# Kernel optimization log

Measured on AMD Instinct MI355X. Metric: run time of the kernel, lower is better.

Reference implementation:

```python
import jax, jax.numpy as jnp
import numpy as np

N, C = 131072, 128
NUM_PREDICTORS = 8


def setup_inputs() -> dict:
    key = jax.random.key(0)
    ks = jax.random.split(key, 9)
    d = {f"outputs{i+1}": jax.random.normal(ks[i], (N, C), dtype=jnp.float32) for i in range(7)}
    d["mimic"] = jax.random.normal(ks[7], (N, C), dtype=jnp.float32)
    d["targets"] = jax.random.randint(ks[8], (N,), 0, C, dtype=jnp.int32)
    d["n_test"] = N
    return d


def _margin(x, targets):
    # x: [N, C]; top-2 margin if the target logit is the max, else 0 (ties by value equality, as in torch code)
    top2, _ = jax.lax.top_k(x, 2)                                  # [N, 2]
    tval = jnp.take_along_axis(x, targets[:, None], axis=1)[:, 0]  # [N]
    return jnp.where(tval == top2[:, 0], top2[:, 0] - top2[:, 1], jnp.zeros((), x.dtype))


def reference(outputs1, outputs2, outputs3, outputs4, outputs5, outputs6, outputs7, mimic, targets, n_test):
    T = 2.0
    preds = [outputs1, outputs2, outputs3, outputs4, outputs5, outputs6, outputs7, mimic]
    # [N, 8] margins, one column per predictor
    margins = jnp.stack([_margin(p, targets) for p in preds], axis=1)
    out_threshold = jax.nn.softmax(margins / T, axis=1)            # softmax over the 8 predictors per sample
    max_preds = jnp.max(jnp.stack(preds[:7], axis=0))              # global max over outputs1..7
    return max_preds, out_threshold
```

## Files before the change

### kernel.cpp

```cpp
#include <hip/hip_runtime.h>
#include <cfloat>

constexpr int kN = 131072;
constexpr int kC = 128;
constexpr int kRows = 16;

__device__ __forceinline__ unsigned fmap(float f) {
    unsigned b = __float_as_uint(f);
    return (b & 0x80000000u) ? ~b : (b | 0x80000000u);
}

__global__ __launch_bounds__(256, 4) void margins_kernel(
    const float* __restrict__ p0, const float* __restrict__ p1,
    const float* __restrict__ p2, const float* __restrict__ p3,
    const float* __restrict__ p4, const float* __restrict__ p5,
    const float* __restrict__ p6, const float* __restrict__ p7,
    const int* __restrict__ targets, float* __restrict__ out,
    unsigned* __restrict__ gmax_ws)
{
    __shared__ float2 P2[8][kRows][34];
    __shared__ float tvbuf[8][17];
    __shared__ float marg[kRows][12];
    __shared__ unsigned blockmax;

    const int t = threadIdx.x;
    const int row0 = blockIdx.x * kRows;
    if (t == 0) blockmax = 0u;

    const float* preds[8] = {p0, p1, p2, p3, p4, p5, p6, p7};

    const int c  = t & 31;
    const int a0 = t >> 5;

#pragma unroll
    for (int it = 0; it < 2; ++it) {
        const int a   = a0 + it * 8;
        const int row = row0 + a;
        const int tgt = targets[row];
        const size_t off = (size_t)row * kC + c * 4;

        float4 v[8];
#pragma unroll
        for (int j = 0; j < 8; ++j) v[j] = *(const float4*)(preds[j] + off);

        const bool hasT = (tgt >> 2) == c;
        const int  ts   = tgt & 3;

#pragma unroll
        for (int j = 0; j < 8; ++j) {
            const float4 w = v[j];
            float a1 = fmaxf(w.x, w.y), a2 = fminf(w.x, w.y);
            float b1 = fmaxf(w.z, w.w), b2 = fminf(w.z, w.w);
            float m1 = fmaxf(a1, b1);
            float m2 = fmaxf(fminf(a1, b1), fmaxf(a2, b2));
            P2[j][a][c] = make_float2(m1, m2);
            if (hasT) {
                float tv = (ts == 0) ? w.x : (ts == 1) ? w.y : (ts == 2) ? w.z : w.w;
                tvbuf[j][a] = tv;
            }
        }
    }
    __syncthreads();

    if (t < 128) {
        const int r = t & 15;
        const int j = t >> 4;
        const float4* pr = (const float4*)(&P2[j][r][0]);
        float m1 = -FLT_MAX, m2 = -FLT_MAX;
#pragma unroll
        for (int k = 0; k < 16; ++k) {
            const float4 q = pr[k];
            float lo = fminf(m1, q.x);
            m1 = fmaxf(m1, q.x);
            m2 = fmaxf(fmaxf(m2, q.y), lo);
            lo = fminf(m1, q.z);
            m1 = fmaxf(m1, q.z);
            m2 = fmaxf(fmaxf(m2, q.w), lo);
        }
        const float tv = tvbuf[j][r];
        marg[r][j] = (tv == m1) ? (m1 - m2) : 0.0f;
        if (j < 7) atomicMax(&blockmax, fmap(m1));
    }
    __syncthreads();

    if (t < 128) {
        const int r  = t >> 3;
        const int jj = t & 7;
        const float4 ma = *(const float4*)&marg[r][0];
        const float4 mb = *(const float4*)&marg[r][4];
        float mm = fmaxf(fmaxf(fmaxf(ma.x, ma.y), fmaxf(ma.z, ma.w)),
                         fmaxf(fmaxf(mb.x, mb.y), fmaxf(mb.z, mb.w)));
        const float e0 = __expf((ma.x - mm) * 0.5f);
        const float e1 = __expf((ma.y - mm) * 0.5f);
        const float e2 = __expf((ma.z - mm) * 0.5f);
        const float e3 = __expf((ma.w - mm) * 0.5f);
        const float e4 = __expf((mb.x - mm) * 0.5f);
        const float e5 = __expf((mb.y - mm) * 0.5f);
        const float e6 = __expf((mb.z - mm) * 0.5f);
        const float e7 = __expf((mb.w - mm) * 0.5f);
        const float s  = e0 + e1 + e2 + e3 + e4 + e5 + e6 + e7;
        float num = (jj == 0) ? e0 : (jj == 1) ? e1 : (jj == 2) ? e2 :
                    (jj == 3) ? e3 : (jj == 4) ? e4 : (jj == 5) ? e5 :
                    (jj == 6) ? e6 : e7;
        out[1 + (size_t)row0 * 8 + t] = num / s;
    }
    if (t == 0) atomicMax(gmax_ws, blockmax);
}

__global__ void finalize_kernel(const unsigned* __restrict__ gmax_ws,
                                float* __restrict__ out)
{
    unsigned u = *gmax_ws;
    unsigned b = (u & 0x80000000u) ? (u & 0x7FFFFFFFu) : ~u;
    out[0] = __uint_as_float(b);
}

extern "C" void kernel_launch(void* const* d_in, const int* in_sizes, int n_in,
                              void* d_out, int out_size, void* d_ws, size_t ws_size,
                              hipStream_t stream) {
    const float* p0 = (const float*)d_in[0];
    const float* p1 = (const float*)d_in[1];
    const float* p2 = (const float*)d_in[2];
    const float* p3 = (const float*)d_in[3];
    const float* p4 = (const float*)d_in[4];
    const float* p5 = (const float*)d_in[5];
    const float* p6 = (const float*)d_in[6];
    const float* p7 = (const float*)d_in[7];
    const int* targets = (const int*)d_in[8];
    float* out = (float*)d_out;
    unsigned* ws = (unsigned*)d_ws;

    hipMemsetAsync(ws, 0, sizeof(unsigned), stream);

    dim3 grid(kN / kRows), block(256);
    margins_kernel<<<grid, block, 0, stream>>>(p0, p1, p2, p3, p4, p5, p6, p7,
                                               targets, out, ws);
    finalize_kernel<<<1, 1, 0, stream>>>(ws, out);
}
```

Baseline: 464.0 us.

## Halve rows per block and spread the top-2 reduction across all threads

Each block now handles 8 rows instead of 16, so every thread loads one row chunk instead of two. The launch-bounds occupancy hint is doubled. The per-(predictor,row) top-2 reduction is split across 4 lanes, combined with xor shuffles. The block max is reduced by wavefront shuffles before a single shared atomic per wave, replacing 112 shared atomics. The aim is more memory-level parallelism and less serialized reduction work, at the cost of twice as many blocks and twice as many global atomics.

```diff
diff --git a/kernel.cpp b/kernel.cpp
--- a/kernel.cpp
+++ b/kernel.cpp
@@ -3,14 +3,14 @@
 
 constexpr int kN = 131072;
 constexpr int kC = 128;
-constexpr int kRows = 16;
+constexpr int kRows = 8;
 
 __device__ __forceinline__ unsigned fmap(float f) {
     unsigned b = __float_as_uint(f);
     return (b & 0x80000000u) ? ~b : (b | 0x80000000u);
 }
 
-__global__ __launch_bounds__(256, 4) void margins_kernel(
+__global__ __launch_bounds__(256, 8) void margins_kernel(
     const float* __restrict__ p0, const float* __restrict__ p1,
     const float* __restrict__ p2, const float* __restrict__ p3,
     const float* __restrict__ p4, const float* __restrict__ p5,
@@ -19,7 +19,7 @@
     unsigned* __restrict__ gmax_ws)
 {
     __shared__ float2 P2[8][kRows][34];
-    __shared__ float tvbuf[8][17];
+    __shared__ float tvbuf[8][kRows + 1];
     __shared__ float marg[kRows][12];
     __shared__ unsigned blockmax;
 
@@ -29,61 +29,73 @@
 
     const float* preds[8] = {p0, p1, p2, p3, p4, p5, p6, p7};
 
-    const int c  = t & 31;
-    const int a0 = t >> 5;
+    const int c = t & 31;
+    const int a = t >> 5;
+    const int row = row0 + a;
+    const int tgt = targets[row];
+    const size_t off = (size_t)row * kC + c * 4;
+
+    float4 v[8];
+#pragma unroll
+    for (int j = 0; j < 8; ++j) v[j] = *(const float4*)(preds[j] + off);
+
+    const bool hasT = (tgt >> 2) == c;
+    const int  ts   = tgt & 3;
 
 #pragma unroll
-    for (int it = 0; it < 2; ++it) {
-        const int a   = a0 + it * 8;
-        const int row = row0 + a;
-        const int tgt = targets[row];
-        const size_t off = (size_t)row * kC + c * 4;
-
-        float4 v[8];
-#pragma unroll
-        for (int j = 0; j < 8; ++j) v[j] = *(const float4*)(preds[j] + off);
-
-        const bool hasT = (tgt >> 2) == c;
-        const int  ts   = tgt & 3;
-
-#pragma unroll
-        for (int j = 0; j < 8; ++j) {
-            const float4 w = v[j];
-            float a1 = fmaxf(w.x, w.y), a2 = fminf(w.x, w.y);
-            float b1 = fmaxf(w.z, w.w), b2 = fminf(w.z, w.w);
-            float m1 = fmaxf(a1, b1);
-            float m2 = fmaxf(fminf(a1, b1), fmaxf(a2, b2));
-            P2[j][a][c] = make_float2(m1, m2);
-            if (hasT) {
-                float tv = (ts == 0) ? w.x : (ts == 1) ? w.y : (ts == 2) ? w.z : w.w;
-                tvbuf[j][a] = tv;
-            }
+    for (int j = 0; j < 8; ++j) {
+        const float4 w = v[j];
+        float a1 = fmaxf(w.x, w.y), a2 = fminf(w.x, w.y);
+        float b1 = fmaxf(w.z, w.w), b2 = fminf(w.z, w.w);
+        float m1 = fmaxf(a1, b1);
+        float m2 = fmaxf(fminf(a1, b1), fmaxf(a2, b2));
+        P2[j][a][c] = make_float2(m1, m2);
+        if (hasT) {
+            tvbuf[j][a] = (ts == 0) ? w.x : (ts == 1) ? w.y : (ts == 2) ? w.z : w.w;
         }
     }
     __syncthreads();
 
-    if (t < 128) {
-        const int r = t & 15;
-        const int j = t >> 4;
-        const float4* pr = (const float4*)(&P2[j][r][0]);
+    {
+        const int u = t >> 2;
+        const int q = t & 3;
+        const int j = u >> 3;
+        const int r = u & 7;
+        const float4* pr = (const float4*)(&P2[j][r][0]) + q * 4;
         float m1 = -FLT_MAX, m2 = -FLT_MAX;
 #pragma unroll
-        for (int k = 0; k < 16; ++k) {
-            const float4 q = pr[k];
-            float lo = fminf(m1, q.x);
-            m1 = fmaxf(m1, q.x);
-            m2 = fmaxf(fmaxf(m2, q.y), lo);
-            lo = fminf(m1, q.z);
-            m1 = fmaxf(m1, q.z);
-            m2 = fmaxf(fmaxf(m2, q.w), lo);
+        for (int k = 0; k < 4; ++k) {
+            const float4 qd = pr[k];
+            float lo = fminf(m1, qd.x);
+            m1 = fmaxf(m1, qd.x);
+            m2 = fmaxf(fmaxf(m2, qd.y), lo);
+            lo = fminf(m1, qd.z);
+            m1 = fmaxf(m1, qd.z);
+            m2 = fmaxf(fmaxf(m2, qd.w), lo);
         }
-        const float tv = tvbuf[j][r];
-        marg[r][j] = (tv == m1) ? (m1 - m2) : 0.0f;
-        if (j < 7) atomicMax(&blockmax, fmap(m1));
+#pragma unroll
+        for (int mask = 1; mask <= 2; mask <<= 1) {
+            const float o1 = __shfl_xor(m1, mask);
+            const float o2 = __shfl_xor(m2, mask);
+            const float lo = fminf(m1, o1);
+            m1 = fmaxf(m1, o1);
+            m2 = fmaxf(fmaxf(m2, o2), lo);
+        }
+        if (q == 0) {
+            const float tv = tvbuf[j][r];
+            marg[r][j] = (tv == m1) ? (m1 - m2) : 0.0f;
+        }
+        unsigned mv = (j < 7) ? fmap(m1) : 0u;
+#pragma unroll
+        for (int mask = 4; mask <= 32; mask <<= 1) {
+            const unsigned o = __shfl_xor(mv, mask);
+            mv = (o > mv) ? o : mv;
+        }
+        if ((t & 63) == 0) atomicMax(&blockmax, mv);
     }
     __syncthreads();
 
-    if (t < 128) {
+    if (t < 64) {
         const int r  = t >> 3;
         const int jj = t & 7;
         const float4 ma = *(const float4*)&marg[r][0];
```

After: 508.3 us. +9.5%, slower.

## Replace shared-memory top-2 reduction with warp shuffles and loop rows per block

Applied to the files above, without the earlier changes.

Each row's top-2 and target value are now reduced across 32 lanes with xor shuffles, and the softmax is computed in registers. This removes the shared-memory staging buffers and the two block barriers. Each block now processes 64 rows over 8 iterations with half the predictors loaded at a time, and the occupancy hint rises to 8 blocks. The global max is reduced per wave before the atomics, so fewer atomic operations are issued. The cost is many more shuffle instructions and fewer loads in flight per iteration on what is a memory-bound stream.

```diff
diff --git a/kernel.cpp b/kernel.cpp
--- a/kernel.cpp
+++ b/kernel.cpp
@@ -3,14 +3,22 @@
 
 constexpr int kN = 131072;
 constexpr int kC = 128;
-constexpr int kRows = 16;
+constexpr int kIters = 8;
+constexpr int kRowsPerIter = 8;
+constexpr int kRowsPerBlock = kIters * kRowsPerIter;
 
 __device__ __forceinline__ unsigned fmap(float f) {
     unsigned b = __float_as_uint(f);
     return (b & 0x80000000u) ? ~b : (b | 0x80000000u);
 }
 
-__global__ __launch_bounds__(256, 4) void margins_kernel(
+__device__ __forceinline__ void top2_merge(float& m1, float& m2, float o1, float o2) {
+    const float lo = fminf(m1, o1);
+    m1 = fmaxf(m1, o1);
+    m2 = fmaxf(fmaxf(m2, o2), lo);
+}
+
+__global__ __launch_bounds__(256, 8) void margins_kernel(
     const float* __restrict__ p0, const float* __restrict__ p1,
     const float* __restrict__ p2, const float* __restrict__ p3,
     const float* __restrict__ p4, const float* __restrict__ p5,
@@ -18,92 +26,75 @@
     const int* __restrict__ targets, float* __restrict__ out,
     unsigned* __restrict__ gmax_ws)
 {
-    __shared__ float2 P2[8][kRows][34];
-    __shared__ float tvbuf[8][17];
-    __shared__ float marg[kRows][12];
     __shared__ unsigned blockmax;
-
     const int t = threadIdx.x;
-    const int row0 = blockIdx.x * kRows;
     if (t == 0) blockmax = 0u;
+    __syncthreads();
 
     const float* preds[8] = {p0, p1, p2, p3, p4, p5, p6, p7};
 
-    const int c  = t & 31;
-    const int a0 = t >> 5;
+    const int c    = t & 31;
+    const int rown = t >> 5;
+    float gm = -FLT_MAX;
 
-#pragma unroll
-    for (int it = 0; it < 2; ++it) {
-        const int a   = a0 + it * 8;
-        const int row = row0 + a;
+    for (int it = 0; it < kIters; ++it) {
+        const int row = blockIdx.x * kRowsPerBlock + it * kRowsPerIter + rown;
         const int tgt = targets[row];
         const size_t off = (size_t)row * kC + c * 4;
 
-        float4 v[8];
-#pragma unroll
-        for (int j = 0; j < 8; ++j) v[j] = *(const float4*)(preds[j] + off);
+        const int ts   = tgt & 3;
+        const int srcl = (t & 32) + (tgt >> 2);
 
-        const bool hasT = (tgt >> 2) == c;
-        const int  ts   = tgt & 3;
+        float marg[8];
 
 #pragma unroll
-        for (int j = 0; j < 8; ++j) {
-            const float4 w = v[j];
-            float a1 = fmaxf(w.x, w.y), a2 = fminf(w.x, w.y);
-            float b1 = fmaxf(w.z, w.w), b2 = fminf(w.z, w.w);
-            float m1 = fmaxf(a1, b1);
-            float m2 = fmaxf(fminf(a1, b1), fmaxf(a2, b2));
-            P2[j][a][c] = make_float2(m1, m2);
-            if (hasT) {
+        for (int h = 0; h < 2; ++h) {
+            float4 v[4];
+#pragma unroll
+            for (int j = 0; j < 4; ++j) v[j] = *(const float4*)(preds[h * 4 + j] + off);
+            __builtin_amdgcn_sched_barrier(0);
+
+#pragma unroll
+            for (int j = 0; j < 4; ++j) {
+                const float4 w = v[j];
+                float a1 = fmaxf(w.x, w.y), a2 = fminf(w.x, w.y);
+                float b1 = fmaxf(w.z, w.w), b2 = fminf(w.z, w.w);
+                float m1 = fmaxf(a1, b1);
+                float m2 = fmaxf(fminf(a1, b1), fmaxf(a2, b2));
                 float tv = (ts == 0) ? w.x : (ts == 1) ? w.y : (ts == 2) ? w.z : w.w;
-                tvbuf[j][a] = tv;
+#pragma unroll
+                for (int mask = 1; mask <= 16; mask <<= 1) {
+                    const float o1 = __shfl_xor(m1, mask);
+                    const float o2 = __shfl_xor(m2, mask);
+                    top2_merge(m1, m2, o1, o2);
+                }
+                tv = __shfl(tv, srcl);
+                marg[h * 4 + j] = (tv == m1) ? (m1 - m2) : 0.0f;
+                if (h * 4 + j < 7) gm = fmaxf(gm, m1);
             }
         }
+
+        const float mm = fmaxf(
+            fmaxf(fmaxf(marg[0], marg[1]), fmaxf(marg[2], marg[3])),
+            fmaxf(fmaxf(marg[4], marg[5]), fmaxf(marg[6], marg[7])));
+        const float e0 = __expf((marg[0] - mm) * 0.5f);
+        const float e1 = __expf((marg[1] - mm) * 0.5f);
+        const float e2 = __expf((marg[2] - mm) * 0.5f);
+        const float e3 = __expf((marg[3] - mm) * 0.5f);
+        const float e4 = __expf((marg[4] - mm) * 0.5f);
+        const float e5 = __expf((marg[5] - mm) * 0.5f);
+        const float e6 = __expf((marg[6] - mm) * 0.5f);
+        const float e7 = __expf((marg[7] - mm) * 0.5f);
+        const float s  = e0 + e1 + e2 + e3 + e4 + e5 + e6 + e7;
+        const float num = (c == 0) ? e0 : (c == 1) ? e1 : (c == 2) ? e2 :
+                          (c == 3) ? e3 : (c == 4) ? e4 : (c == 5) ? e5 :
+                          (c == 6) ? e6 : e7;
+        if (c < 8) out[1 + (size_t)row * 8 + c] = num / s;
     }
+
+    gm = fmaxf(gm, __shfl_xor(gm, 32));
+    if ((t & 63) == 0) atomicMax(&blockmax, fmap(gm));
     __syncthreads();
-
-    if (t < 128) {
-        const int r = t & 15;
-        const int j = t >> 4;
-        const float4* pr = (const float4*)(&P2[j][r][0]);
-        float m1 = -FLT_MAX, m2 = -FLT_MAX;
-#pragma unroll
-        for (int k = 0; k < 16; ++k) {
-            const float4 q = pr[k];
-            float lo = fminf(m1, q.x);
-            m1 = fmaxf(m1, q.x);
-            m2 = fmaxf(fmaxf(m2, q.y), lo);
-            lo = fminf(m1, q.z);
-            m1 = fmaxf(m1, q.z);
-            m2 = fmaxf(fmaxf(m2, q.w), lo);
-        }
-        const float tv = tvbuf[j][r];
-        marg[r][j] = (tv == m1) ? (m1 - m2) : 0.0f;
-        if (j < 7) atomicMax(&blockmax, fmap(m1));
-    }
-    __syncthreads();
-
-    if (t < 128) {
-        const int r  = t >> 3;
-        const int jj = t & 7;
-        const float4 ma = *(const float4*)&marg[r][0];
-        const float4 mb = *(const float4*)&marg[r][4];
-        float mm = fmaxf(fmaxf(fmaxf(ma.x, ma.y), fmaxf(ma.z, ma.w)),
-                         fmaxf(fmaxf(mb.x, mb.y), fmaxf(mb.z, mb.w)));
-        const float e0 = __expf((ma.x - mm) * 0.5f);
-        const float e1 = __expf((ma.y - mm) * 0.5f);
-        const float e2 = __expf((ma.z - mm) * 0.5f);
-        const float e3 = __expf((ma.w - mm) * 0.5f);
-        const float e4 = __expf((mb.x - mm) * 0.5f);
-        const float e5 = __expf((mb.y - mm) * 0.5f);
-        const float e6 = __expf((mb.z - mm) * 0.5f);
-        const float e7 = __expf((mb.w - mm) * 0.5f);
-        const float s  = e0 + e1 + e2 + e3 + e4 + e5 + e6 + e7;
-        float num = (jj == 0) ? e0 : (jj == 1) ? e1 : (jj == 2) ? e2 :
-                    (jj == 3) ? e3 : (jj == 4) ? e4 : (jj == 5) ? e5 :
-                    (jj == 6) ? e6 : e7;
-        out[1 + (size_t)row0 * 8 + t] = num / s;
-    }
     if (t == 0) atomicMax(gmax_ws, blockmax);
 }
 
@@ -132,7 +123,7 @@
 
     hipMemsetAsync(ws, 0, sizeof(unsigned), stream);
 
-    dim3 grid(kN / kRows), block(256);
+    dim3 grid(kN / kRowsPerBlock), block(256);
     margins_kernel<<<grid, block, 0, stream>>>(p0, p1, p2, p3, p4, p5, p6, p7,
                                                targets, out, ws);
     finalize_kernel<<<1, 1, 0, stream>>>(ws, out);
```

Measured after the change: 474.7 us. 2.3% more time.
